# Optimization experiments

Hardware: AMD Instinct MI355X
Metric: run time of the kernel (lower is better)

## Reference

```python
import jax, jax.numpy as jnp
import numpy as np

D = 256   # model dim
M = 64    # num mechanisms
B = 4
S = 8192


def setup_inputs() -> dict:
    key = jax.random.key(0)
    ks = jax.random.split(key, 16)
    n = jax.random.normal
    inp = {
        "x": n(ks[0], (B, S, D), jnp.float32),
        "context": n(ks[1], (B, S, D), jnp.float32),
        # stacked per-mechanism params (m, out, in) etc.
        "Wm": n(ks[2], (M, D, D), jnp.float32) * (1.0 / np.sqrt(D)),
        "bm": n(ks[3], (M, D), jnp.float32) * 0.02,
        "cm": n(ks[4], (M, D), jnp.float32),           # characteristics (1,1,dim) per node
        "um": n(ks[5], (M, D), jnp.float32) * (1.0 / np.sqrt(D)),  # timing_gate weight
        "vm": n(ks[6], (M,), jnp.float32) * 0.02,       # timing_gate bias
        # selector: Linear(d, 2d) -> GELU -> Linear(2d, m)
        "W1": n(ks[7], (2 * D, D), jnp.float32) * (1.0 / np.sqrt(D)),
        "b1": n(ks[8], (2 * D,), jnp.float32) * 0.02,
        "W2": n(ks[9], (M, 2 * D), jnp.float32) * (1.0 / np.sqrt(2 * D)),
        "b2": n(ks[10], (M,), jnp.float32) * 0.02,
        # integrate: Linear(2d, d)
        "Wi": n(ks[11], (D, 2 * D), jnp.float32) * (1.0 / np.sqrt(2 * D)),
        "bi": n(ks[12], (D,), jnp.float32) * 0.02,
    }
    return inp


def reference(x, context, Wm, bm, cm, um, vm, W1, b1, W2, b2, Wi, bi):
    # selector: softmax over mechanisms (b, s, m)
    h = jax.nn.gelu(jnp.einsum('bsd,ed->bse', context, W1) + b1, approximate=False)
    scores = jax.nn.softmax(jnp.einsum('bse,me->bsm', h, W2) + b2, axis=-1)

    # per-mechanism sigmoid timing gate (b, s, m)
    gate = jax.nn.sigmoid(jnp.einsum('bsd,md->bsm', x, um) + vm)

    # combined weight a[b,s,m] = softmax_score * gate; then
    # selected = sum_m a * (x @ Wm.T + bm + cm)  -- contracted without
    # materializing the (b, s, m, d) stack the torch loop builds.
    a = scores * gate                               # (b, s, m)
    selected = jnp.einsum('bsm,bse,mde->bsd', a, x, Wm) \
             + jnp.einsum('bsm,md->bsd', a, bm + cm)

    # integrate(concat([x, selected]))
    cat = jnp.concatenate([x, selected], axis=-1)   # (b, s, 2d)
    integrated = jnp.einsum('bse,de->bsd', cat, Wi) + bi
    return integrated
```

## Files before the change

### kernel.cpp

```cpp
#include <hip/hip_runtime.h>
#include <cstdint>
#include <cstddef>


typedef _Float16 f16;
typedef f16 f16x8 __attribute__((ext_vector_type(8)));
typedef float f32x4 __attribute__((ext_vector_type(4)));

#define DEV __device__ __forceinline__

DEV uint32_t swz128(uint32_t b) { return b ^ (((b >> 7) & 7u) << 4); }

DEV void gload_lds16(const void* g, void* l) {
  __builtin_amdgcn_global_load_lds(
      (const __attribute__((address_space(1))) unsigned int*)g,
      (__attribute__((address_space(3))) unsigned int*)l, 16, 0, 0);
}

DEV f16x8 cvt8(float4 u0, float4 u1) {
  f16x8 v = {(f16)u0.x, (f16)u0.y, (f16)u0.z, (f16)u0.w,
             (f16)u1.x, (f16)u1.y, (f16)u1.z, (f16)u1.w};
  return v;
}

__global__ void prep_b_kernel(const float* __restrict__ S, f16* __restrict__ dst,
                              int K, int BN, int total) {
  int t = blockIdx.x * 256 + threadIdx.x;
  if (t >= total) return;
  int gpc = BN * 8;
  int g = t % gpc;
  int c = (t / gpc) % (K / 64);
  int cb = t / (gpc * (K / 64));
  int ks = g / (BN * 4);
  int rem = g % (BN * 4);
  int col = rem >> 2;
  int kg = rem & 3;
  int J = cb * BN + col;
  int k = c * 64 + ks * 32 + kg * 8;
  const float* s = S + (size_t)J * K + k;
  float4 u0 = *(const float4*)s;
  float4 u1 = *(const float4*)(s + 4);
  f16* chunk = dst + (size_t)(cb * (K / 64) + c) * (BN * 64);
  *(f16x8*)((char*)chunk + swz128((uint32_t)g * 16)) = cvt8(u0, u1);
}

__global__ void prep_wcat_kernel(const float* __restrict__ Wm,
                                 const float* __restrict__ bm,
                                 const float* __restrict__ cm,
                                 f16* __restrict__ dst) {
  int t = blockIdx.x * 256 + threadIdx.x;
  if (t >= 257 * 2048) return;
  int g = t & 2047;
  int c = t >> 11;
  int ks = g >> 10;
  int rem = g & 1023;
  int col = rem >> 2;
  int kg = rem & 3;
  int k0 = ks * 32 + kg * 8;
  f16x8 v;
  if (c < 256) {
    int m = c & 63;
    int e0 = (c >> 6) * 64 + k0;
    const float* s = Wm + ((size_t)m * 256 + col) * 256 + e0;
    float4 u0 = *(const float4*)s;
    float4 u1 = *(const float4*)(s + 4);
    v = cvt8(u0, u1);
  } else {
#pragma unroll
    for (int j = 0; j < 8; ++j) {
      int k = k0 + j;
      v[j] = (f16)(bm[k * 256 + col] + cm[k * 256 + col]);
    }
  }
  *(f16x8*)((char*)(dst + (size_t)c * 16384) + swz128((uint32_t)g * 16)) = v;
}

template <int BN, int NCHUNK, int A0C, int EPI>
__global__ __launch_bounds__(BN == 256 ? 512 : 256, 2)
void gemm_tpl(const float* __restrict__ A0, int lda0,
              const f16* __restrict__ A1, int lda1,
              const f16* __restrict__ Bt,
              const float* __restrict__ bias,
              float* __restrict__ outF, f16* __restrict__ outH, int ldo) {
  constexpr int WAVES = (BN == 256) ? 8 : 4;
  constexpr int THREADS = WAVES * 64;
  constexpr int WC = (BN == 256) ? 4 : 1;
  constexpr int WR = WAVES / WC;
  constexpr int RT = 128 / (WR * 16);
  constexpr int CT = (BN / WC) / 16;

  __shared__ alignas(16) f16 sA[2][128 * 64];
  __shared__ alignas(16) f16 sB[2][BN * 64];

  const int tid = threadIdx.x;
  const int lane = tid & 63;
  const int wid = tid >> 6;
  const int wr = wid / WC, wc = wid % WC;
  const int rb = blockIdx.x, cb = blockIdx.y;

  auto stageB = [&](int c, int buf) {
    const char* src = (const char*)(Bt + (size_t)(cb * NCHUNK + c) * (BN * 64));
#pragma unroll
    for (int it = 0; it < (BN * 64 * 2) / (THREADS * 16); ++it) {
      int off = (it * THREADS + tid) * 16;
      gload_lds16(src + off, (char*)&sB[buf][0] + off);
    }
  };
  auto stageA = [&](int c, int buf) {
#pragma unroll
    for (int it = 0; it < 1024 / THREADS; ++it) {
      int gg = it * THREADS + tid;
      int row = gg >> 3, eg = gg & 7;
      size_t rowG = (size_t)rb * 128 + row;
      f16x8 v;
      if (A0C > 0 && c < A0C) {
        const float* s = A0 + rowG * lda0 + c * 64 + eg * 8;
        float4 u0 = *(const float4*)s;
        float4 u1 = *(const float4*)(s + 4);
        v = cvt8(u0, u1);
      } else {
        v = *(const f16x8*)(A1 + rowG * lda1 + (c - A0C) * 64 + eg * 8);
      }
      *(f16x8*)((char*)&sA[buf][0] + swz128((uint32_t)(row * 128 + eg * 16))) = v;
    }
  };

  f32x4 acc[RT][CT];
#pragma unroll
  for (int i = 0; i < RT; ++i)
#pragma unroll
    for (int j = 0; j < CT; ++j) acc[i][j] = (f32x4){0.f, 0.f, 0.f, 0.f};

  stageB(0, 0);
  stageA(0, 0);
  __syncthreads();

  for (int c = 0; c < NCHUNK; ++c) {
    int cur = c & 1;
    if (c + 1 < NCHUNK) {
      stageB(c + 1, cur ^ 1);
      stageA(c + 1, cur ^ 1);
    }
#pragma unroll
    for (int ks = 0; ks < 2; ++ks) {
      f16x8 af[RT], bf[CT];
#pragma unroll
      for (int rt = 0; rt < RT; ++rt) {
        int row = wr * (RT * 16) + rt * 16 + (lane & 15);
        af[rt] = *(const f16x8*)((const char*)&sA[cur][0] +
                                 swz128((uint32_t)(row * 128 + ks * 64 + (lane >> 4) * 16)));
      }
#pragma unroll
      for (int ct = 0; ct < CT; ++ct) {
        int col = wc * (CT * 16) + ct * 16 + (lane & 15);
        bf[ct] = *(const f16x8*)((const char*)&sB[cur][0] +
                                 swz128((uint32_t)(((ks * BN + col) * 4 + (lane >> 4)) * 16)));
      }
#pragma unroll
      for (int rt = 0; rt < RT; ++rt)
#pragma unroll
        for (int ct = 0; ct < CT; ++ct)
          acc[rt][ct] = __builtin_amdgcn_mfma_f32_16x16x32_f16(af[rt], bf[ct], acc[rt][ct], 0, 0, 0);
    }
    __syncthreads();
  }

#pragma unroll
  for (int rt = 0; rt < RT; ++rt)
#pragma unroll
    for (int ct = 0; ct < CT; ++ct)
#pragma unroll
      for (int i = 0; i < 4; ++i) {
        size_t row = (size_t)rb * 128 + wr * (RT * 16) + rt * 16 + (lane >> 4) * 4 + i;
        int colG = cb * BN + wc * (CT * 16) + ct * 16 + (lane & 15);
        float v = acc[rt][ct][i];
        if constexpr (EPI == 0) {
          if (bias) v += bias[colG];
          outF[row * ldo + colG] = v;
        } else {
          v += bias[colG];
          float ge = 0.5f * v * (1.0f + erff(v * 0.70710678118f));
          outH[row * ldo + colG] = (f16)ge;
        }
      }
}

__global__ void selector_finish(const float* __restrict__ logits,
                                const float* __restrict__ glog,
                                const float* __restrict__ b2,
                                const float* __restrict__ vm,
                                f16* __restrict__ a16) {
  int n = blockIdx.x * 4 + (threadIdx.x >> 6);
  int m = threadIdx.x & 63;
  float l = logits[(size_t)n * 64 + m] + b2[m];
  float mx = l;
#pragma unroll
  for (int o = 32; o; o >>= 1) mx = fmaxf(mx, __shfl_xor(mx, o));
  float p = expf(l - mx);
  float s = p;
#pragma unroll
  for (int o = 32; o; o >>= 1) s += __shfl_xor(s, o);
  float g = glog[(size_t)n * 64 + m] + vm[m];
  float gate = 1.0f / (1.0f + expf(-g));
  a16[(size_t)n * 64 + m] = (f16)(p / s * gate);
}

__global__ __launch_bounds__(512, 2)
void big_gemm(const float* __restrict__ x, const f16* __restrict__ a16,
              const f16* __restrict__ Wcat, f16* __restrict__ sel) {
  __shared__ alignas(16) f16 sB[4][256 * 64];
  __shared__ alignas(16) f16 sAa[128 * 72];

  const int tid = threadIdx.x;
  const int lane = tid & 63;
  const int wid = tid >> 6;
  const int wr = wid >> 2, wc = wid & 3;
  const int rb = blockIdx.x;
  const int row0 = wr * 64 + (lane & 15);
  const int ksub = lane >> 4;

  auto stageB = [&](int c, int buf) {
    const char* src = (const char*)(Wcat + (size_t)c * 16384);
#pragma unroll
    for (int it = 0; it < 4; ++it) {
      int off = (it * 512 + tid) * 16;
      gload_lds16(src + off, (char*)&sB[buf][0] + off);
    }
  };

#pragma unroll
  for (int it = 0; it < 2; ++it) {
    int gg = it * 512 + tid;
    int row = gg >> 3, mg = gg & 7;
    f16x8 v = *(const f16x8*)(a16 + ((size_t)rb * 128 + row) * 64 + mg * 8);
    *(f16x8*)((char*)sAa + row * 144 + mg * 16) = v;
  }
  stageB(0, 0);
  stageB(1, 1);
  stageB(2, 2);
  asm volatile("s_waitcnt lgkmcnt(0)" ::: "memory");
  __builtin_amdgcn_s_barrier();

  f32x4 acc[4][4];
#pragma unroll
  for (int i = 0; i < 4; ++i)
#pragma unroll
    for (int j = 0; j < 4; ++j) acc[i][j] = (f32x4){0.f, 0.f, 0.f, 0.f};

  f16x8 xv[2][4];
  auto loadXV = [&](int er) {
#pragma unroll
    for (int ks = 0; ks < 2; ++ks)
#pragma unroll
      for (int rt = 0; rt < 4; ++rt) {
        const float* s = x + ((size_t)rb * 128 + row0 + rt * 16) * 256
                           + er * 64 + ks * 32 + ksub * 8;
        float4 u0 = *(const float4*)s;
        float4 u1 = *(const float4*)(s + 4);
        xv[ks][rt] = cvt8(u0, u1);
      }
  };

  for (int q8 = 0; q8 < 256; q8 += 8) {
    if ((q8 & 63) == 0) loadXV(q8 >> 6);
    f16x8 as8[4];
#pragma unroll
    for (int rt = 0; rt < 4; ++rt)
      as8[rt] = *(const f16x8*)((const char*)sAa + (row0 + rt * 16) * 144 + (q8 & 63) * 2);
#pragma unroll
    for (int u = 0; u < 8; ++u) {
      const int q = q8 + u;
      asm volatile("s_waitcnt vmcnt(8)" ::: "memory");
      __builtin_amdgcn_s_barrier();
      stageB(q + 3, (q + 3) & 3);
      const char* bbase = (const char*)&sB[q & 3][0];
#pragma unroll
      for (int ks = 0; ks < 2; ++ks) {
        f16x8 bf[4];
#pragma unroll
        for (int ct = 0; ct < 4; ++ct) {
          int col = wc * 64 + ct * 16 + (lane & 15);
          bf[ct] = *(const f16x8*)(bbase +
                     swz128((uint32_t)(((ks * 256 + col) * 4 + ksub) * 16)));
        }
        f16x8 af[4];
#pragma unroll
        for (int rt = 0; rt < 4; ++rt) af[rt] = xv[ks][rt] * as8[rt][u];
        __builtin_amdgcn_s_setprio(1);
#pragma unroll
        for (int rt = 0; rt < 4; ++rt)
#pragma unroll
          for (int ct = 0; ct < 4; ++ct)
            acc[rt][ct] = __builtin_amdgcn_mfma_f32_16x16x32_f16(af[rt], bf[ct], acc[rt][ct], 0, 0, 0);
        __builtin_amdgcn_s_setprio(0);
      }
    }
  }

  asm volatile("s_waitcnt vmcnt(8)" ::: "memory");
  __builtin_amdgcn_s_barrier();
#pragma unroll
  for (int ks = 0; ks < 2; ++ks) {
    f16x8 af[4], bf[4];
#pragma unroll
    for (int rt = 0; rt < 4; ++rt)
      af[rt] = *(const f16x8*)((const char*)sAa + (row0 + rt * 16) * 144 + ks * 64 + ksub * 16);
#pragma unroll
    for (int ct = 0; ct < 4; ++ct) {
      int col = wc * 64 + ct * 16 + (lane & 15);
      bf[ct] = *(const f16x8*)((const char*)&sB[0][0] +
                 swz128((uint32_t)(((ks * 256 + col) * 4 + ksub) * 16)));
    }
#pragma unroll
    for (int rt = 0; rt < 4; ++rt)
#pragma unroll
      for (int ct = 0; ct < 4; ++ct)
        acc[rt][ct] = __builtin_amdgcn_mfma_f32_16x16x32_f16(af[rt], bf[ct], acc[rt][ct], 0, 0, 0);
  }

#pragma unroll
  for (int rt = 0; rt < 4; ++rt)
#pragma unroll
    for (int ct = 0; ct < 4; ++ct)
#pragma unroll
      for (int i = 0; i < 4; ++i) {
        size_t row = (size_t)rb * 128 + wr * 64 + rt * 16 + (lane >> 4) * 4 + i;
        int col = wc * 64 + ct * 16 + (lane & 15);
        sel[row * 256 + col] = (f16)acc[rt][ct][i];
      }
}

extern "C" void kernel_launch(void* const* d_in, const int* in_sizes, int n_in,
                              void* d_out, int out_size, void* d_ws, size_t ws_size,
                              hipStream_t stream) {
  (void)in_sizes; (void)n_in; (void)out_size;
  const float* x   = (const float*)d_in[0];
  const float* ctx = (const float*)d_in[1];
  const float* Wm  = (const float*)d_in[2];
  const float* bm  = (const float*)d_in[3];
  const float* cm  = (const float*)d_in[4];
  const float* um  = (const float*)d_in[5];
  const float* vm  = (const float*)d_in[6];
  const float* W1  = (const float*)d_in[7];
  const float* b1  = (const float*)d_in[8];
  const float* W2  = (const float*)d_in[9];
  const float* b2  = (const float*)d_in[10];
  const float* Wi  = (const float*)d_in[11];
  const float* bi  = (const float*)d_in[12];
  float* out = (float*)d_out;

  char* ws = (char*)d_ws;
  size_t off = 0;
  f16* Wcat = (f16*)(ws + off); off += (size_t)260 * 16384 * 2;
  f16* W1t  = (f16*)(ws + off); off += (size_t)512 * 256 * 2;
  f16* W2t  = (f16*)(ws + off); off += (size_t)64 * 512 * 2;
  f16* umt  = (f16*)(ws + off); off += (size_t)64 * 256 * 2;
  f16* Wit  = (f16*)(ws + off); off += (size_t)256 * 512 * 2;
  f16* h16  = (f16*)(ws + off); off += (size_t)32768 * 512 * 2;
  float* logits = (float*)(ws + off); off += (size_t)32768 * 64 * 4;
  float* glog   = (float*)(ws + off); off += (size_t)32768 * 64 * 4;
  f16* a16   = (f16*)(ws + off); off += (size_t)32768 * 64 * 2;
  f16* sel16 = (f16*)(ws + off); off += (size_t)32768 * 256 * 2;
  if (ws_size < off) return;

  prep_wcat_kernel<<<dim3(257 * 2048 / 256), dim3(256), 0, stream>>>(Wm, bm, cm, Wcat);
  prep_b_kernel<<<dim3(16384 / 256), dim3(256), 0, stream>>>(W1, W1t, 256, 256, 16384);
  prep_b_kernel<<<dim3(4096 / 256),  dim3(256), 0, stream>>>(W2, W2t, 512, 64, 4096);
  prep_b_kernel<<<dim3(2048 / 256),  dim3(256), 0, stream>>>(um, umt, 256, 64, 2048);
  prep_b_kernel<<<dim3(16384 / 256), dim3(256), 0, stream>>>(Wi, Wit, 512, 256, 16384);

  gemm_tpl<256, 4, 4, 1><<<dim3(256, 2), dim3(512), 0, stream>>>(
      ctx, 256, nullptr, 0, W1t, b1, nullptr, h16, 512);
  gemm_tpl<64, 4, 4, 0><<<dim3(256, 1), dim3(256), 0, stream>>>(
      x, 256, nullptr, 0, umt, nullptr, glog, nullptr, 64);
  gemm_tpl<64, 8, 0, 0><<<dim3(256, 1), dim3(256), 0, stream>>>(
      nullptr, 0, h16, 512, W2t, nullptr, logits, nullptr, 64);
  selector_finish<<<dim3(32768 / 4), dim3(256), 0, stream>>>(logits, glog, b2, vm, a16);

  big_gemm<<<dim3(256), dim3(512), 0, stream>>>(x, a16, Wcat, sel16);

  gemm_tpl<256, 8, 4, 0><<<dim3(256, 1), dim3(512), 0, stream>>>(
      x, 256, sel16, 256, Wit, bi, out, nullptr, 256);
}
```

Before: 344.1 us.

## Switch big_gemm to 32x32x16 MFMA with per-wave column tiles and register-prefetched B

Rewrites the main mechanism-contraction GEMM to use 32x32x16 MFMA instructions. Each wave now owns a 32-column strip across all 128 rows instead of a 64x64 tile. The Wcat layout is repacked without swizzle to match the new fragment order, and B fragments are double-buffered in registers, loaded one stage ahead. The waitcnt depth is adjusted and sched barriers are added. The aim is fewer LDS reads per MFMA and better instruction overlap, at the cost of redundant x loads per wave (each wave loads all 128 rows) and possible LDS bank conflicts without swizzle.

```diff
diff --git a/kernel.cpp b/kernel.cpp
--- a/kernel.cpp
+++ b/kernel.cpp
@@ -6,6 +6,7 @@
 typedef _Float16 f16;
 typedef f16 f16x8 __attribute__((ext_vector_type(8)));
 typedef float f32x4 __attribute__((ext_vector_type(4)));
+typedef float f32x16 __attribute__((ext_vector_type(16)));
 
 #define DEV __device__ __forceinline__
 
@@ -52,11 +53,10 @@
   if (t >= 257 * 2048) return;
   int g = t & 2047;
   int c = t >> 11;
-  int ks = g >> 10;
-  int rem = g & 1023;
-  int col = rem >> 2;
-  int kg = rem & 3;
-  int k0 = ks * 32 + kg * 8;
+  int kstep = g >> 9;
+  int khalf = (g >> 8) & 1;
+  int col = g & 255;
+  int k0 = kstep * 16 + khalf * 8;
   f16x8 v;
   if (c < 256) {
     int m = c & 63;
@@ -72,7 +72,7 @@
       v[j] = (f16)(bm[k * 256 + col] + cm[k * 256 + col]);
     }
   }
-  *(f16x8*)((char*)(dst + (size_t)c * 16384) + swz128((uint32_t)g * 16)) = v;
+  *(f16x8*)(dst + (size_t)c * 16384 + (size_t)g * 8) = v;
 }
 
 template <int BN, int NCHUNK, int A0C, int EPI>
@@ -214,10 +214,9 @@
   const int tid = threadIdx.x;
   const int lane = tid & 63;
   const int wid = tid >> 6;
-  const int wr = wid >> 2, wc = wid & 3;
+  const int l31 = lane & 31;
+  const int khalf = lane >> 5;
   const int rb = blockIdx.x;
-  const int row0 = wr * 64 + (lane & 15);
-  const int ksub = lane >> 4;
 
   auto stageB = [&](int c, int buf) {
     const char* src = (const char*)(Wcat + (size_t)c * 16384);
@@ -238,96 +237,85 @@
   stageB(0, 0);
   stageB(1, 1);
   stageB(2, 2);
-  asm volatile("s_waitcnt lgkmcnt(0)" ::: "memory");
+  asm volatile("s_waitcnt vmcnt(8) lgkmcnt(0)" ::: "memory");
   __builtin_amdgcn_s_barrier();
-
-  f32x4 acc[4][4];
-#pragma unroll
-  for (int i = 0; i < 4; ++i)
-#pragma unroll
-    for (int j = 0; j < 4; ++j) acc[i][j] = (f32x4){0.f, 0.f, 0.f, 0.f};
-
-  f16x8 xv[2][4];
+  __builtin_amdgcn_sched_barrier(0);
+
+  f32x16 acc[4];
+#pragma unroll
+  for (int rt = 0; rt < 4; ++rt)
+#pragma unroll
+    for (int r = 0; r < 16; ++r) acc[rt][r] = 0.f;
+
+  f16x8 xv[4][4];
   auto loadXV = [&](int er) {
 #pragma unroll
-    for (int ks = 0; ks < 2; ++ks)
-#pragma unroll
-      for (int rt = 0; rt < 4; ++rt) {
-        const float* s = x + ((size_t)rb * 128 + row0 + rt * 16) * 256
-                           + er * 64 + ks * 32 + ksub * 8;
+    for (int rt = 0; rt < 4; ++rt)
+#pragma unroll
+      for (int ks = 0; ks < 4; ++ks) {
+        const float* s = x + ((size_t)rb * 128 + rt * 32 + l31) * 256
+                           + er * 64 + ks * 16 + khalf * 8;
         float4 u0 = *(const float4*)s;
         float4 u1 = *(const float4*)(s + 4);
-        xv[ks][rt] = cvt8(u0, u1);
+        xv[rt][ks] = cvt8(u0, u1);
       }
   };
+
+  const int bOff = khalf * 4096 + wid * 512 + l31 * 16;
+
+  f16x8 bf[2][4];
+#pragma unroll
+  for (int ks = 0; ks < 4; ++ks)
+    bf[0][ks] = *(const f16x8*)((const char*)&sB[0][0] + bOff + ks * 8192);
 
   for (int q8 = 0; q8 < 256; q8 += 8) {
     if ((q8 & 63) == 0) loadXV(q8 >> 6);
     f16x8 as8[4];
 #pragma unroll
     for (int rt = 0; rt < 4; ++rt)
-      as8[rt] = *(const f16x8*)((const char*)sAa + (row0 + rt * 16) * 144 + (q8 & 63) * 2);
+      as8[rt] = *(const f16x8*)((const char*)sAa + (rt * 32 + l31) * 144 + (q8 & 63) * 2);
 #pragma unroll
     for (int u = 0; u < 8; ++u) {
       const int q = q8 + u;
-      asm volatile("s_waitcnt vmcnt(8)" ::: "memory");
+      asm volatile("s_waitcnt vmcnt(4)" ::: "memory");
       __builtin_amdgcn_s_barrier();
-      stageB(q + 3, (q + 3) & 3);
-      const char* bbase = (const char*)&sB[q & 3][0];
-#pragma unroll
-      for (int ks = 0; ks < 2; ++ks) {
-        f16x8 bf[4];
-#pragma unroll
-        for (int ct = 0; ct < 4; ++ct) {
-          int col = wc * 64 + ct * 16 + (lane & 15);
-          bf[ct] = *(const f16x8*)(bbase +
-                     swz128((uint32_t)(((ks * 256 + col) * 4 + ksub) * 16)));
+      __builtin_amdgcn_sched_barrier(0);
+      stageB(q + 3, (u + 3) & 3);
+      const char* nb = (const char*)&sB[(u + 1) & 3][0] + bOff;
+#pragma unroll
+      for (int ks = 0; ks < 4; ++ks)
+        bf[(u + 1) & 1][ks] = *(const f16x8*)(nb + ks * 8192);
+      __builtin_amdgcn_s_setprio(1);
+#pragma unroll
+      for (int ks = 0; ks < 4; ++ks) {
+#pragma unroll
+        for (int rt = 0; rt < 4; ++rt) {
+          f16x8 af = xv[rt][ks] * as8[rt][u];
+          acc[rt] = __builtin_amdgcn_mfma_f32_32x32x16_f16(af, bf[u & 1][ks], acc[rt], 0, 0, 0);
         }
-        f16x8 af[4];
-#pragma unroll
-        for (int rt = 0; rt < 4; ++rt) af[rt] = xv[ks][rt] * as8[rt][u];
-        __builtin_amdgcn_s_setprio(1);
-#pragma unroll
-        for (int rt = 0; rt < 4; ++rt)
-#pragma unroll
-          for (int ct = 0; ct < 4; ++ct)
-            acc[rt][ct] = __builtin_amdgcn_mfma_f32_16x16x32_f16(af[rt], bf[ct], acc[rt][ct], 0, 0, 0);
-        __builtin_amdgcn_s_setprio(0);
-      }
-    }
-  }
-
-  asm volatile("s_waitcnt vmcnt(8)" ::: "memory");
-  __builtin_amdgcn_s_barrier();
-#pragma unroll
-  for (int ks = 0; ks < 2; ++ks) {
-    f16x8 af[4], bf[4];
-#pragma unroll
-    for (int rt = 0; rt < 4; ++rt)
-      af[rt] = *(const f16x8*)((const char*)sAa + (row0 + rt * 16) * 144 + ks * 64 + ksub * 16);
-#pragma unroll
-    for (int ct = 0; ct < 4; ++ct) {
-      int col = wc * 64 + ct * 16 + (lane & 15);
-      bf[ct] = *(const f16x8*)((const char*)&sB[0][0] +
-                 swz128((uint32_t)(((ks * 256 + col) * 4 + ksub) * 16)));
-    }
-#pragma unroll
-    for (int rt = 0; rt < 4; ++rt)
-#pragma unroll
-      for (int ct = 0; ct < 4; ++ct)
-        acc[rt][ct] = __builtin_amdgcn_mfma_f32_16x16x32_f16(af[rt], bf[ct], acc[rt][ct], 0, 0, 0);
+      }
+      __builtin_amdgcn_s_setprio(0);
+    }
+  }
+
+#pragma unroll
+  for (int ks = 0; ks < 4; ++ks) {
+#pragma unroll
+    for (int rt = 0; rt < 4; ++rt) {
+      f16x8 af = *(const f16x8*)((const char*)sAa + (rt * 32 + l31) * 144
+                                 + ks * 32 + khalf * 16);
+      acc[rt] = __builtin_amdgcn_mfma_f32_32x32x16_f16(af, bf[0][ks], acc[rt], 0, 0, 0);
+    }
   }
 
 #pragma unroll
   for (int rt = 0; rt < 4; ++rt)
 #pragma unroll
-    for (int ct = 0; ct < 4; ++ct)
-#pragma unroll
-      for (int i = 0; i < 4; ++i) {
-        size_t row = (size_t)rb * 128 + wr * 64 + rt * 16 + (lane >> 4) * 4 + i;
-        int col = wc * 64 + ct * 16 + (lane & 15);
-        sel[row * 256 + col] = (f16)acc[rt][ct][i];
-      }
+    for (int r = 0; r < 16; ++r) {
+      int rowin = (r & 3) + 8 * (r >> 2) + 4 * khalf;
+      size_t row = (size_t)rb * 128 + rt * 32 + rowin;
+      sel[row * 256 + wid * 32 + l31] = (f16)acc[rt][r];
+    }
 }
 
 extern "C" void kernel_launch(void* const* d_in, const int* in_sizes, int n_in,
```

New measurement: 388.0 us. +12.8%, slower.
